# Optimization experiments

Measured on AMD Instinct MI355X. Metric: run time of the kernel, lower is better.

The kernel has to match this reference:

```python
import jax, jax.numpy as jnp
import numpy as np

D_MODEL = 1024
N_HEADS = 16
HEAD_DIM = D_MODEL // N_HEADS
NEG_INF = -1e9


def setup_inputs() -> dict:
    key = jax.random.key(0)
    ks = jax.random.split(key, 12)
    B, S = 2, 2048
    std = 1.0 / np.sqrt(D_MODEL)
    def lin(k):
        kw, kb = jax.random.split(k)
        W = jax.random.uniform(kw, (D_MODEL, D_MODEL), jnp.float32, -std, std)
        b = jax.random.uniform(kb, (D_MODEL,), jnp.float32, -std, std)
        return W, b
    Wq, bq = lin(ks[0])
    Wk, bk = lin(ks[1])
    Wv, bv = lin(ks[2])
    Wo, bo = lin(ks[3])
    Q = jax.random.normal(ks[4], (B, S, D_MODEL), jnp.float32)
    K = jax.random.normal(ks[5], (B, S, D_MODEL), jnp.float32)
    V = jax.random.normal(ks[6], (B, S, D_MODEL), jnp.float32)
    # causal attention mask: True means masked (disallowed)
    attn_mask = jnp.triu(jnp.ones((S, S), dtype=bool), k=1)
    padding_mask = jnp.zeros((B, S), dtype=bool)  # no padding
    return {"Q": Q, "K": K, "V": V, "attn_mask": attn_mask,
            "padding_mask": padding_mask,
            "Wq": Wq, "bq": bq, "Wk": Wk, "bk": bk,
            "Wv": Wv, "bv": bv, "Wo": Wo, "bo": bo}


def reference(Q, K, V, attn_mask, padding_mask, Wq, bq, Wk, bk, Wv, bv, Wo, bo):
    B, Sq, _ = Q.shape
    Sk = K.shape[1]
    # QKV projections, split into heads -> [B, H, S, Dh]
    def proj(x, W, b):
        y = x @ W.T + b
        return y.reshape(B, -1, N_HEADS, HEAD_DIM).transpose(0, 2, 1, 3)
    q = proj(Q, Wq, bq)
    k = proj(K, Wk, bk)
    v = proj(V, Wv, bv)
    # scaled dot-product attention (dropout is identity in eval mode)
    scores = jnp.einsum('bhqd,bhkd->bhqk', q, k) / jnp.sqrt(
        jnp.asarray(HEAD_DIM, q.dtype))
    mask = attn_mask[None, None, :, :] | padding_mask[:, None, None, :]
    scores = jnp.where(mask, NEG_INF, scores)
    attn = jax.nn.softmax(scores, axis=-1)
    x = jnp.einsum('bhqk,bhkd->bhqd', attn, v)
    x = x.transpose(0, 2, 1, 3).reshape(B, Sq, D_MODEL)
    return x @ Wo.T + bo
```

## Files before the change

kernel.cpp:

```cpp
#include <hip/hip_runtime.h>
#include <hip/hip_bf16.h>
#include <cstddef>
#include <cstdint>

#define S_LEN  2048
#define DMODEL 1024
#define NHEADS 16

typedef __attribute__((ext_vector_type(8))) short  short8;
typedef __attribute__((ext_vector_type(4))) short  s16x4;
typedef __attribute__((ext_vector_type(8))) __bf16 bf16x8;
typedef __attribute__((ext_vector_type(4))) float  f32x4;

__device__ __forceinline__ f32x4 MFMA(short8 a, short8 b, f32x4 c) {
    return __builtin_amdgcn_mfma_f32_16x16x32_bf16(
        __builtin_bit_cast(bf16x8, a), __builtin_bit_cast(bf16x8, b), c, 0, 0, 0);
}

__device__ __forceinline__ unsigned short f2bs(float f) {
    return __builtin_bit_cast(unsigned short, __float2bfloat16(f));
}
__device__ __forceinline__ float bs2f(unsigned short u) {
    unsigned int x = ((unsigned int)u) << 16;
    return __builtin_bit_cast(float, x);
}

__device__ __forceinline__ short8 cvt8(f32x4 a, f32x4 b) {
    short8 r;
#pragma unroll
    for (int i = 0; i < 4; ++i) {
        r[i]     = (short)f2bs(a[i]);
        r[4 + i] = (short)f2bs(b[i]);
    }
    return r;
}

__device__ __forceinline__ short8 scale8(short8 v) {
    short8 r;
#pragma unroll
    for (int i = 0; i < 8; ++i)
        r[i] = (short)f2bs(bs2f((unsigned short)v[i]) * 0.125f);
    return r;
}

__device__ __forceinline__ int xcd_swz(int bid, int nwg) {
    const int chunk = nwg >> 3;
    return (bid & 7) * chunk + (bid >> 3);
}

__device__ __forceinline__ void bar_sync() {
    asm volatile("s_waitcnt lgkmcnt(0)" ::: "memory");
    __builtin_amdgcn_sched_barrier(0);
    __builtin_amdgcn_s_barrier();
}

__global__ __launch_bounds__(256)
void wcvt(const float* __restrict__ Wq, const float* __restrict__ Wk,
          const float* __restrict__ Wv, unsigned short* __restrict__ wb)
{
    const int i = blockIdx.x * 256 + threadIdx.x;
    const float* src = (i < 131072) ? Wq : (i < 262144) ? Wk : Wv;
    const size_t j = (size_t)(i & 131071) * 8;
    const short8 v = cvt8(((const f32x4*)(src + j))[0], ((const f32x4*)(src + j))[1]);
    *(short8*)(wb + (size_t)i * 8) = v;
}

template<bool HEADSPLIT, bool WBF16>
struct StageRegs {
    f32x4  af[2][2];
    short8 ab[2];
    f32x4  wf[2][2];
    short8 wb[2];
};

template<bool HEADSPLIT, bool WBF16>
__device__ __forceinline__ void gemm_body(const void* __restrict__ Ap,
                                          const void* __restrict__ Wp,
                                          const float* __restrict__ bias,
                                          void* __restrict__ outp,
                                          int m0, int n0)
{
    __shared__ short a_lds[2][128 * 32];
    __shared__ short w_lds[2][128 * 32];
    const int t    = threadIdx.x;
    const int lane = t & 63;
    const int wid  = t >> 6;
    const int wr   = (wid >> 1) << 6;
    const int wc   = (wid & 1) << 6;
    const int fr   = lane & 15;
    const int ks   = lane >> 4;

    const int row0 = t >> 2,         sl0 = t & 3;
    const int row1 = (256 + t) >> 2, sl1 = (256 + t) & 3;
    const int ms0  = sl0 ^ ((row0 >> 1) & 3);
    const int ms1  = sl1 ^ ((row1 >> 1) & 3);

    using SR = StageRegs<HEADSPLIT, WBF16>;
    SR S0, S1;

    auto load_stage = [&](SR& S, int k0) {
        if constexpr (HEADSPLIT) {
            const float* A = (const float*)Ap;
            const float* pa0 = A + (size_t)(m0 + row0) * DMODEL + k0 + sl0 * 8;
            S.af[0][0] = ((const f32x4*)pa0)[0]; S.af[0][1] = ((const f32x4*)pa0)[1];
            const float* pa1 = A + (size_t)(m0 + row1) * DMODEL + k0 + sl1 * 8;
            S.af[1][0] = ((const f32x4*)pa1)[0]; S.af[1][1] = ((const f32x4*)pa1)[1];
        } else {
            const unsigned short* A = (const unsigned short*)Ap;
            S.ab[0] = *(const short8*)(A + (size_t)(m0 + row0) * DMODEL + k0 + sl0 * 8);
            S.ab[1] = *(const short8*)(A + (size_t)(m0 + row1) * DMODEL + k0 + sl1 * 8);
        }
        if constexpr (WBF16) {
            const unsigned short* Wb = (const unsigned short*)Wp;
            S.wb[0] = *(const short8*)(Wb + (size_t)(n0 + row0) * DMODEL + k0 + sl0 * 8);
            S.wb[1] = *(const short8*)(Wb + (size_t)(n0 + row1) * DMODEL + k0 + sl1 * 8);
        } else {
            const float* W = (const float*)Wp;
            const float* pw0 = W + (size_t)(n0 + row0) * DMODEL + k0 + sl0 * 8;
            S.wf[0][0] = ((const f32x4*)pw0)[0]; S.wf[0][1] = ((const f32x4*)pw0)[1];
            const float* pw1 = W + (size_t)(n0 + row1) * DMODEL + k0 + sl1 * 8;
            S.wf[1][0] = ((const f32x4*)pw1)[0]; S.wf[1][1] = ((const f32x4*)pw1)[1];
        }
    };

    auto store_stage = [&](const SR& S, int buf) {
        if constexpr (HEADSPLIT) {
            *(short8*)&a_lds[buf][row0 * 32 + ms0 * 8] = cvt8(S.af[0][0], S.af[0][1]);
            *(short8*)&a_lds[buf][row1 * 32 + ms1 * 8] = cvt8(S.af[1][0], S.af[1][1]);
        } else {
            *(short8*)&a_lds[buf][row0 * 32 + ms0 * 8] = S.ab[0];
            *(short8*)&a_lds[buf][row1 * 32 + ms1 * 8] = S.ab[1];
        }
        if constexpr (WBF16) {
            *(short8*)&w_lds[buf][row0 * 32 + ms0 * 8] = S.wb[0];
            *(short8*)&w_lds[buf][row1 * 32 + ms1 * 8] = S.wb[1];
        } else {
            *(short8*)&w_lds[buf][row0 * 32 + ms0 * 8] = cvt8(S.wf[0][0], S.wf[0][1]);
            *(short8*)&w_lds[buf][row1 * 32 + ms1 * 8] = cvt8(S.wf[1][0], S.wf[1][1]);
        }
    };

    f32x4 acc[4][4] = {};

    auto compute = [&](int cur) {
        short8 af[4], bfr[4];
#pragma unroll
        for (int i = 0; i < 4; ++i) {
            const int ra = wr + i * 16 + fr;
            af[i]  = *(const short8*)&a_lds[cur][ra * 32 + ((ks ^ ((ra >> 1) & 3)) << 3)];
            const int rb = wc + i * 16 + fr;
            bfr[i] = *(const short8*)&w_lds[cur][rb * 32 + ((ks ^ ((rb >> 1) & 3)) << 3)];
        }
#pragma unroll
        for (int mi = 0; mi < 4; ++mi)
#pragma unroll
            for (int ni = 0; ni < 4; ++ni)
                acc[mi][ni] = MFMA(af[mi], bfr[ni], acc[mi][ni]);
    };

    load_stage(S0, 0);
    store_stage(S0, 0);
    load_stage(S1, 32);
    bar_sync();

    for (int tt = 0; tt < 32; tt += 2) {
        if (tt + 2 < 32) load_stage(S0, (tt + 2) * 32);
        compute(0);
        if (tt + 1 < 32) store_stage(S1, 1);
        bar_sync();
        if (tt + 3 < 32) load_stage(S1, (tt + 3) * 32);
        compute(1);
        if (tt + 2 < 32) store_stage(S0, 0);
        if (tt + 2 < 32) bar_sync();
    }

#pragma unroll
    for (int ni = 0; ni < 4; ++ni) {
        const int n    = n0 + wc + ni * 16 + fr;
        const float bv = bias[n];
#pragma unroll
        for (int mi = 0; mi < 4; ++mi) {
#pragma unroll
            for (int j = 0; j < 4; ++j) {
                const int m = m0 + wr + mi * 16 + ks * 4 + j;
                const float val = acc[mi][ni][j] + bv;
                if constexpr (HEADSPLIT) {
                    const int b = m >> 11, s = m & (S_LEN - 1);
                    const int hh = n >> 6, dh = n & 63;
                    ((unsigned short*)outp)[((((size_t)b * NHEADS + hh) * S_LEN + s) << 6) + dh]
                        = f2bs(val);
                } else {
                    ((float*)outp)[(size_t)m * DMODEL + n] = val;
                }
            }
        }
    }
}

__global__ __launch_bounds__(256, 3)
void qkv_gemm(const float* __restrict__ Q, const float* __restrict__ K,
              const float* __restrict__ V,
              const unsigned short* __restrict__ wb,
              const float* __restrict__ bq, const float* __restrict__ bk,
              const float* __restrict__ bv,
              unsigned short* qh, unsigned short* kh, unsigned short* vh)
{
    const int swz = xcd_swz(blockIdx.x, 768);
    const int z   = swz >> 8;
    const int rem = swz & 255;
    const int my  = rem >> 3;
    const int nx  = rem & 7;
    const float *A, *B; unsigned short* O;
    if (z == 0)      { A = Q; B = bq; O = qh; }
    else if (z == 1) { A = K; B = bk; O = kh; }
    else             { A = V; B = bv; O = vh; }
    gemm_body<true, true>(A, wb + ((size_t)z << 20), B, O, my * 128, nx * 128);
}

__global__ __launch_bounds__(256, 3)
void out_gemm(const unsigned short* __restrict__ X, const float* __restrict__ Wo,
              const float* __restrict__ bo, float* __restrict__ out)
{
    const int swz = xcd_swz(blockIdx.x, 256);
    gemm_body<false, false>(X, Wo, bo, out, (swz >> 3) * 128, (swz & 7) * 128);
}

#define VSTR 72
#define PSTR 88

struct QState {
    short8 qf0, qf1;
    f32x4  oacc[4];
    float  m, l;
    int    qr0;
};

__device__ __forceinline__ void attn_tile(QState& st, const int k0,
                                          const short* k_lds, const short* v_lds,
                                          short* p_buf, const int fr, const int ks)
{
    const int myq = st.qr0 + fr;
    f32x4 sacc[4] = {};
    __builtin_amdgcn_s_setprio(1);
#pragma unroll
    for (int nk = 0; nk < 4; ++nk) {
        const int rb = nk * 16 + fr;
        short8 a0 = *(const short8*)&k_lds[rb * 64 + (((ks)     ^ (rb & 7)) << 3)];
        short8 a1 = *(const short8*)&k_lds[rb * 64 + (((4 + ks) ^ (rb & 7)) << 3)];
        sacc[nk] = MFMA(a0, st.qf0, sacc[nk]);
        sacc[nk] = MFMA(a1, st.qf1, sacc[nk]);
    }
    __builtin_amdgcn_s_setprio(0);

    float mx = -1e9f;
    if (k0 + 63 <= st.qr0) {
#pragma unroll
        for (int nk = 0; nk < 4; ++nk)
#pragma unroll
            for (int jj = 0; jj < 4; ++jj) mx = fmaxf(mx, sacc[nk][jj]);
    } else {
#pragma unroll
        for (int nk = 0; nk < 4; ++nk)
#pragma unroll
            for (int jj = 0; jj < 4; ++jj) {
                const int key = k0 + nk * 16 + ks * 4 + jj;
                float s = (key <= myq) ? sacc[nk][jj] : -1e9f;
                sacc[nk][jj] = s;
                mx = fmaxf(mx, s);
            }
    }
    mx = fmaxf(mx, __shfl_xor(mx, 16));
    mx = fmaxf(mx, __shfl_xor(mx, 32));
    if (!__all(mx <= st.m + 8.f)) {
        const float mnew = fmaxf(st.m, mx);
        const float corr = __expf(st.m - mnew);
        st.m = mnew;
        st.l *= corr;
#pragma unroll
        for (int nd = 0; nd < 4; ++nd)
#pragma unroll
            for (int jj = 0; jj < 4; ++jj) st.oacc[nd][jj] *= corr;
    }

    float rsum = 0.f;
#pragma unroll
    for (int nk = 0; nk < 4; ++nk) {
        s16x4 pw;
#pragma unroll
        for (int jj = 0; jj < 4; ++jj) {
            const float p = __expf(sacc[nk][jj] - st.m);
            rsum += p;
            pw[jj] = (short)f2bs(p);
        }
        *(s16x4*)&p_buf[fr * PSTR + nk * 16 + ks * 4] = pw;
    }
    rsum += __shfl_xor(rsum, 16);
    rsum += __shfl_xor(rsum, 32);
    st.l += rsum;
    asm volatile("" ::: "memory");

    __builtin_amdgcn_s_setprio(1);
#pragma unroll
    for (int sh = 0; sh < 2; ++sh) {
        short8 pa = *(const short8*)&p_buf[fr * PSTR + sh * 32 + ks * 8];
#pragma unroll
        for (int nd = 0; nd < 4; ++nd) {
            short8 vf = *(const short8*)&v_lds[(nd * 16 + fr) * VSTR + sh * 32 + ks * 8];
            st.oacc[nd] = MFMA(vf, pa, st.oacc[nd]);
        }
    }
    __builtin_amdgcn_s_setprio(0);
}

__global__ __launch_bounds__(256, 2)
void attn_kernel(const unsigned short* __restrict__ qh,
                 const unsigned short* __restrict__ kh,
                 const unsigned short* __restrict__ vh,
                 unsigned short* __restrict__ xh)
{
    __shared__ short k_lds[64 * 64];
    __shared__ short v_lds[64 * VSTR];
    __shared__ short p_lds[4][16 * PSTR];

    const int t    = threadIdx.x;
    const int lane = t & 63;
    const int wid  = t >> 6;
    const int fr   = lane & 15;
    const int ks   = lane >> 4;
    const int swz  = xcd_swz(blockIdx.x, 512);
    const int bh   = swz >> 4;
    const int xp   = swz & 15;
    const int qa0  = xp * 64;
    const int qb0  = (31 - xp) * 64;
    const int ntA  = xp + 1;
    const int ntB  = 32 - xp;

    const unsigned short* qb_ = qh + ((size_t)bh << 17);
    const unsigned short* kb  = kh + ((size_t)bh << 17);
    const unsigned short* vb  = vh + ((size_t)bh << 17);

    QState A, B;
    A.qr0 = qa0 + wid * 16;  B.qr0 = qb0 + wid * 16;
    A.qf0 = scale8(*(const short8*)&qb_[(A.qr0 + fr) * 64 + ks * 8]);
    A.qf1 = scale8(*(const short8*)&qb_[(A.qr0 + fr) * 64 + 32 + ks * 8]);
    B.qf0 = scale8(*(const short8*)&qb_[(B.qr0 + fr) * 64 + ks * 8]);
    B.qf1 = scale8(*(const short8*)&qb_[(B.qr0 + fr) * 64 + 32 + ks * 8]);
#pragma unroll
    for (int nd = 0; nd < 4; ++nd) { A.oacc[nd] = f32x4{}; B.oacc[nd] = f32x4{}; }
    A.m = B.m = -1e9f; A.l = B.l = 0.f;

    short8 kv[2], vv[2];
#pragma unroll
    for (int cc = 0; cc < 2; ++cc) {
        const int c   = cc * 256 + t;
        const int row = c >> 3;
        const int sl  = c & 7;
        kv[cc] = *(const short8*)(kb + (size_t)row * 64 + sl * 8);
        const int key = c & 63;
        const int d0  = (c >> 6) * 8;
        vv[cc] = *(const short8*)(vb + (size_t)key * 64 + d0);
    }

    for (int kt = 0; kt < ntB; ++kt) {
        const int k0 = kt * 64;
        bar_sync();

#pragma unroll
        for (int cc = 0; cc < 2; ++cc) {
            const int c   = cc * 256 + t;
            const int row = c >> 3;
            const int ms  = (c & 7) ^ (row & 7);
            *(short8*)&k_lds[row * 64 + ms * 8] = kv[cc];
            const int key = c & 63;
            const int d0  = (c >> 6) * 8;
#pragma unroll
            for (int i = 0; i < 8; ++i)
                v_lds[(d0 + i) * VSTR + key] = vv[cc][i];
        }
        bar_sync();

        if (kt + 1 < ntB) {
            const int k1 = k0 + 64;
#pragma unroll
            for (int cc = 0; cc < 2; ++cc) {
                const int c   = cc * 256 + t;
                const int row = c >> 3;
                const int sl  = c & 7;
                kv[cc] = *(const short8*)(kb + (size_t)(k1 + row) * 64 + sl * 8);
                const int key = c & 63;
                const int d0  = (c >> 6) * 8;
                vv[cc] = *(const short8*)(vb + (size_t)(k1 + key) * 64 + d0);
            }
        }

        attn_tile(B, k0, k_lds, v_lds, p_lds[wid], fr, ks);
        if (kt < ntA)
            attn_tile(A, k0, k_lds, v_lds, p_lds[wid], fr, ks);
    }

    const int b = bh >> 4, h = bh & 15;
#pragma unroll
    for (int which = 0; which < 2; ++which) {
        QState& st = which ? B : A;
        const float inv = 1.f / st.l;
        const size_t base = ((size_t)b * S_LEN + (st.qr0 + fr)) * DMODEL + h * 64;
#pragma unroll
        for (int nd = 0; nd < 4; ++nd)
#pragma unroll
            for (int jj = 0; jj < 4; ++jj)
                xh[base + nd * 16 + ks * 4 + jj] = f2bs(st.oacc[nd][jj] * inv);
    }
}

extern "C" void kernel_launch(void* const* d_in, const int* in_sizes, int n_in,
                              void* d_out, int out_size, void* d_ws, size_t ws_size,
                              hipStream_t stream)
{
    const float* Q  = (const float*)d_in[0];
    const float* K  = (const float*)d_in[1];
    const float* V  = (const float*)d_in[2];
    const float* Wq = (const float*)d_in[5];
    const float* bq = (const float*)d_in[6];
    const float* Wk = (const float*)d_in[7];
    const float* bk = (const float*)d_in[8];
    const float* Wv = (const float*)d_in[9];
    const float* bv = (const float*)d_in[10];
    const float* Wo = (const float*)d_in[11];
    const float* bo = (const float*)d_in[12];
    float* out = (float*)d_out;

    const size_t HSZ = (size_t)2 * S_LEN * DMODEL;
    unsigned short* qh = (unsigned short*)d_ws;
    unsigned short* kh = qh + HSZ;
    unsigned short* vh = kh + HSZ;
    unsigned short* xh = vh + HSZ;
    unsigned short* wb = xh;

    wcvt<<<1536, 256, 0, stream>>>(Wq, Wk, Wv, wb);
    qkv_gemm<<<768, 256, 0, stream>>>(Q, K, V, wb, bq, bk, bv, qh, kh, vh);
    attn_kernel<<<512, 256, 0, stream>>>(qh, kh, vh, xh);
    out_gemm<<<256, 256, 0, stream>>>(xh, Wo, bo, out);
}
```

Baseline: 123.0 us.

## Load bf16 GEMM operand directly to LDS via global_load_lds

In both projection GEMMs, the operand already in bf16 (weights for QKV, attention output for the output GEMM) is now copied straight from global memory into swizzled LDS with global_load_lds. Only the fp32 operand still goes through registers for conversion. This aims to cut register pressure and VGPR-to-LDS store instructions, and to overlap the direct loads with compute. The pipeline is restructured with explicit vmcnt waits and a peeled final iteration, which depends on getting the outstanding-load counting right.

Result: faster. 118.9 us (-3.3%).

```diff
diff --git a/kernel.cpp b/kernel.cpp
--- a/kernel.cpp
+++ b/kernel.cpp
@@ -53,6 +53,10 @@
     __builtin_amdgcn_sched_barrier(0);
     __builtin_amdgcn_s_barrier();
 }
+
+#define GLDS16(src, dst) __builtin_amdgcn_global_load_lds( \
+    (__attribute__((address_space(1))) void*)(src),        \
+    (__attribute__((address_space(3))) void*)(dst), 16, 0, 0)
 
 __global__ __launch_bounds__(256)
 void wcvt(const float* __restrict__ Wq, const float* __restrict__ Wk,
@@ -65,15 +69,9 @@
     *(short8*)(wb + (size_t)i * 8) = v;
 }
 
-template<bool HEADSPLIT, bool WBF16>
-struct StageRegs {
-    f32x4  af[2][2];
-    short8 ab[2];
-    f32x4  wf[2][2];
-    short8 wb[2];
-};
-
-template<bool HEADSPLIT, bool WBF16>
+struct FS { f32x4 v[2][2]; };
+
+template<bool A_F32>
 __device__ __forceinline__ void gemm_body(const void* __restrict__ Ap,
                                           const void* __restrict__ Wp,
                                           const float* __restrict__ bias,
@@ -95,49 +93,35 @@
     const int ms0  = sl0 ^ ((row0 >> 1) & 3);
     const int ms1  = sl1 ^ ((row1 >> 1) & 3);
 
-    using SR = StageRegs<HEADSPLIT, WBF16>;
-    SR S0, S1;
-
-    auto load_stage = [&](SR& S, int k0) {
-        if constexpr (HEADSPLIT) {
-            const float* A = (const float*)Ap;
-            const float* pa0 = A + (size_t)(m0 + row0) * DMODEL + k0 + sl0 * 8;
-            S.af[0][0] = ((const f32x4*)pa0)[0]; S.af[0][1] = ((const f32x4*)pa0)[1];
-            const float* pa1 = A + (size_t)(m0 + row1) * DMODEL + k0 + sl1 * 8;
-            S.af[1][0] = ((const f32x4*)pa1)[0]; S.af[1][1] = ((const f32x4*)pa1)[1];
-        } else {
-            const unsigned short* A = (const unsigned short*)Ap;
-            S.ab[0] = *(const short8*)(A + (size_t)(m0 + row0) * DMODEL + k0 + sl0 * 8);
-            S.ab[1] = *(const short8*)(A + (size_t)(m0 + row1) * DMODEL + k0 + sl1 * 8);
-        }
-        if constexpr (WBF16) {
-            const unsigned short* Wb = (const unsigned short*)Wp;
-            S.wb[0] = *(const short8*)(Wb + (size_t)(n0 + row0) * DMODEL + k0 + sl0 * 8);
-            S.wb[1] = *(const short8*)(Wb + (size_t)(n0 + row1) * DMODEL + k0 + sl1 * 8);
-        } else {
-            const float* W = (const float*)Wp;
-            const float* pw0 = W + (size_t)(n0 + row0) * DMODEL + k0 + sl0 * 8;
-            S.wf[0][0] = ((const f32x4*)pw0)[0]; S.wf[0][1] = ((const f32x4*)pw0)[1];
-            const float* pw1 = W + (size_t)(n0 + row1) * DMODEL + k0 + sl1 * 8;
-            S.wf[1][0] = ((const f32x4*)pw1)[0]; S.wf[1][1] = ((const f32x4*)pw1)[1];
-        }
+    const int g0 = wid * 2, g1 = g0 + 1;
+    const int gsl   = lane & 3;
+    const int grow0 = g0 * 16 + (lane >> 2);
+    const int grow1 = g1 * 16 + (lane >> 2);
+    const int ssl0  = gsl ^ ((grow0 >> 1) & 3);
+    const int ssl1  = gsl ^ ((grow1 >> 1) & 3);
+
+    const float* Rp             = (const float*)(A_F32 ? Ap : Wp);
+    const unsigned short* Gp    = (const unsigned short*)(A_F32 ? Wp : Ap);
+    const int rbase             = A_F32 ? m0 : n0;
+    const int gbase             = A_F32 ? n0 : m0;
+    short (*r_lds)[128 * 32]    = A_F32 ? a_lds : w_lds;
+    short (*g_lds)[128 * 32]    = A_F32 ? w_lds : a_lds;
+
+    auto load_R = [&](FS& S, int k0) {
+        const float* p0 = Rp + (size_t)(rbase + row0) * DMODEL + k0 + sl0 * 8;
+        S.v[0][0] = ((const f32x4*)p0)[0]; S.v[0][1] = ((const f32x4*)p0)[1];
+        const float* p1 = Rp + (size_t)(rbase + row1) * DMODEL + k0 + sl1 * 8;
+        S.v[1][0] = ((const f32x4*)p1)[0]; S.v[1][1] = ((const f32x4*)p1)[1];
     };
-
-    auto store_stage = [&](const SR& S, int buf) {
-        if constexpr (HEADSPLIT) {
-            *(short8*)&a_lds[buf][row0 * 32 + ms0 * 8] = cvt8(S.af[0][0], S.af[0][1]);
-            *(short8*)&a_lds[buf][row1 * 32 + ms1 * 8] = cvt8(S.af[1][0], S.af[1][1]);
-        } else {
-            *(short8*)&a_lds[buf][row0 * 32 + ms0 * 8] = S.ab[0];
-            *(short8*)&a_lds[buf][row1 * 32 + ms1 * 8] = S.ab[1];
-        }
-        if constexpr (WBF16) {
-            *(short8*)&w_lds[buf][row0 * 32 + ms0 * 8] = S.wb[0];
-            *(short8*)&w_lds[buf][row1 * 32 + ms1 * 8] = S.wb[1];
-        } else {
-            *(short8*)&w_lds[buf][row0 * 32 + ms0 * 8] = cvt8(S.wf[0][0], S.wf[0][1]);
-            *(short8*)&w_lds[buf][row1 * 32 + ms1 * 8] = cvt8(S.wf[1][0], S.wf[1][1]);
-        }
+    auto store_R = [&](const FS& S, int buf) {
+        *(short8*)&r_lds[buf][row0 * 32 + ms0 * 8] = cvt8(S.v[0][0], S.v[0][1]);
+        *(short8*)&r_lds[buf][row1 * 32 + ms1 * 8] = cvt8(S.v[1][0], S.v[1][1]);
+    };
+    auto gload_G = [&](int k0, int buf) {
+        GLDS16(Gp + (size_t)(gbase + grow0) * DMODEL + k0 + ssl0 * 8,
+               &g_lds[buf][g0 * 512]);
+        GLDS16(Gp + (size_t)(gbase + grow1) * DMODEL + k0 + ssl1 * 8,
+               &g_lds[buf][g1 * 512]);
     };
 
     f32x4 acc[4][4] = {};
@@ -158,21 +142,33 @@
                 acc[mi][ni] = MFMA(af[mi], bfr[ni], acc[mi][ni]);
     };
 
-    load_stage(S0, 0);
-    store_stage(S0, 0);
-    load_stage(S1, 32);
+    FS SA, SB;
+    gload_G(0, 0);
+    load_R(SA, 0);
+    store_R(SA, 0);
+    load_R(SB, 32);
     bar_sync();
 
-    for (int tt = 0; tt < 32; tt += 2) {
-        if (tt + 2 < 32) load_stage(S0, (tt + 2) * 32);
+    for (int tt = 0; tt < 30; tt += 2) {
+        gload_G((tt + 1) * 32, 1);
+        load_R(SA, (tt + 2) * 32);
         compute(0);
-        if (tt + 1 < 32) store_stage(S1, 1);
+        store_R(SB, 1);
+        asm volatile("s_waitcnt vmcnt(4)" ::: "memory");
         bar_sync();
-        if (tt + 3 < 32) load_stage(S1, (tt + 3) * 32);
+        gload_G((tt + 2) * 32, 0);
+        load_R(SB, (tt + 3) * 32);
         compute(1);
-        if (tt + 2 < 32) store_stage(S0, 0);
-        if (tt + 2 < 32) bar_sync();
-    }
+        store_R(SA, 0);
+        asm volatile("s_waitcnt vmcnt(4)" ::: "memory");
+        bar_sync();
+    }
+    gload_G(31 * 32, 1);
+    compute(0);
+    store_R(SB, 1);
+    asm volatile("s_waitcnt vmcnt(0)" ::: "memory");
+    bar_sync();
+    compute(1);
 
 #pragma unroll
     for (int ni = 0; ni < 4; ++ni) {
@@ -184,7 +180,7 @@
             for (int j = 0; j < 4; ++j) {
                 const int m = m0 + wr + mi * 16 + ks * 4 + j;
                 const float val = acc[mi][ni][j] + bv;
-                if constexpr (HEADSPLIT) {
+                if constexpr (A_F32) {
                     const int b = m >> 11, s = m & (S_LEN - 1);
                     const int hh = n >> 6, dh = n & 63;
                     ((unsigned short*)outp)[((((size_t)b * NHEADS + hh) * S_LEN + s) << 6) + dh]
@@ -214,7 +210,7 @@
     if (z == 0)      { A = Q; B = bq; O = qh; }
     else if (z == 1) { A = K; B = bk; O = kh; }
     else             { A = V; B = bv; O = vh; }
-    gemm_body<true, true>(A, wb + ((size_t)z << 20), B, O, my * 128, nx * 128);
+    gemm_body<true>(A, wb + ((size_t)z << 20), B, O, my * 128, nx * 128);
 }
 
 __global__ __launch_bounds__(256, 3)
@@ -222,7 +218,7 @@
               const float* __restrict__ bo, float* __restrict__ out)
 {
     const int swz = xcd_swz(blockIdx.x, 256);
-    gemm_body<false, false>(X, Wo, bo, out, (swz >> 3) * 128, (swz & 7) * 128);
+    gemm_body<false>(X, Wo, bo, out, (swz >> 3) * 128, (swz & 7) * 128);
 }
 
 #define VSTR 72
```
